# Performance work log

Hardware: AMD Instinct MI355X
Metric: run time of the kernel (lower is better)

The kernel has to match this reference:

```python
import jax, jax.numpy as jnp
import numpy as np

B, S, D, H = 4, 1024, 1024, 16
DH = D // H


def setup_inputs() -> dict:
    key = jax.random.key(0)
    ks = jax.random.split(key, 9)
    s = 0.02
    return {
        "x": jax.random.normal(ks[0], (B, S, D), dtype=jnp.float32),
        "mask": jax.random.randint(ks[1], (B, 1, S), 0, 2, dtype=jnp.int32),
        "Wq": jax.random.normal(ks[2], (D, D), dtype=jnp.float32) * s,
        "bq": jnp.zeros((D,), dtype=jnp.float32),
        "Wk": jax.random.normal(ks[3], (D, D), dtype=jnp.float32) * s,
        "Wv": jax.random.normal(ks[4], (D, D), dtype=jnp.float32) * s,
        "bv": jnp.zeros((D,), dtype=jnp.float32),
        "Wo": jax.random.normal(ks[5], (D, D), dtype=jnp.float32) * s,
        "bo": jnp.zeros((D,), dtype=jnp.float32),
    }


def reference(x, mask, Wq, bq, Wk, Wv, bv, Wo, bo):
    # Linear projections (torch Linear: y = x @ W.T + b)
    q = x @ Wq.T + bq
    k = x @ Wk.T  # key has bias=False
    v = x @ Wv.T + bv

    scale = jnp.asarray(DH, x.dtype) ** (-0.25)
    # [B,S,D] -> [B,H,S,DH]
    qh = q.reshape(B, S, H, DH).transpose(0, 2, 1, 3) * scale
    kh = k.reshape(B, S, H, DH).transpose(0, 2, 1, 3) * scale
    vh = v.reshape(B, S, H, DH).transpose(0, 2, 1, 3)

    qk = jnp.einsum("bhqd,bhkd->bhqk", qh, kh)  # [B,H,S,S]

    # pad-mask branch: mask [B,1,S] -> [B,1,1,S], 0 means padded
    pad = (mask == 0)[:, :, None, :]
    min_value = jnp.finfo(qk.dtype).min
    qk = jnp.where(pad, min_value, qk)

    qk = qk.astype(jnp.float32)
    w = jax.nn.softmax(qk, axis=-1).astype(x.dtype)
    w = jnp.where(pad, jnp.asarray(0.0, w.dtype), w)

    wv = jnp.einsum("bhqk,bhkd->bhqd", w, vh)  # [B,H,S,DH]
    wv = wv.transpose(0, 2, 1, 3).reshape(B, S, D)
    out = wv @ Wo.T + bo
    return out, jax.lax.stop_gradient(qk)
```

## Files before the change

kernel.cpp:

```cpp
#include <hip/hip_runtime.h>

#define NB 4
#define NS 1024
#define ND 1024
#define NH 16
#define NDH 64

typedef __attribute__((ext_vector_type(8))) short short8;
typedef __attribute__((ext_vector_type(4))) short s16x4;
typedef __attribute__((ext_vector_type(4))) float f32x4;

#define SENT (-3.3895313892515355e38f)

static __device__ __forceinline__ unsigned short f2bf(float f) {
    unsigned u = __builtin_bit_cast(unsigned, f);
    u += 0x7fffu + ((u >> 16) & 1u);
    return (unsigned short)(u >> 16);
}

static __device__ __forceinline__ f32x4 mfma16(short8 a, short8 b, f32x4 c) {
    return __builtin_amdgcn_mfma_f32_16x16x32_bf16(a, b, c, 0, 0, 0);
}

typedef const __attribute__((address_space(1))) unsigned int gu32_t;
typedef __attribute__((address_space(3))) unsigned int su32_t;
#define GLOAD_LDS16(gp, lp) \
    __builtin_amdgcn_global_load_lds((gu32_t*)(const void*)(gp), (su32_t*)(void*)(lp), 16, 0, 0)

__global__ __launch_bounds__(256) void cast_to_bf16(
    const float* __restrict__ x,  const float* __restrict__ wq,
    const float* __restrict__ wk, const float* __restrict__ wv,
    const float* __restrict__ wo, short* __restrict__ xb,
    short* __restrict__ wqb, short* __restrict__ wkb,
    short* __restrict__ wvb, short* __restrict__ wob)
{
    int i = blockIdx.x * 256 + threadIdx.x;
    const float* s; short* d; int off;
    const int XQ = 1 << 20, WQ = 1 << 18;
    if (i < XQ)               { s = x;  d = xb;  off = i; }
    else if (i < XQ + WQ)     { s = wq; d = wqb; off = i - XQ; }
    else if (i < XQ + 2 * WQ) { s = wk; d = wkb; off = i - XQ - WQ; }
    else if (i < XQ + 3 * WQ) { s = wv; d = wvb; off = i - XQ - 2 * WQ; }
    else                      { s = wo; d = wob; off = i - XQ - 3 * WQ; }
    float4 v = ((const float4*)s)[off];
    s16x4 r = { (short)f2bf(v.x), (short)f2bf(v.y), (short)f2bf(v.z), (short)f2bf(v.w) };
    ((s16x4*)d)[off] = r;
}

__global__ __launch_bounds__(256) void gemm_qkv(
    const short* __restrict__ X, const short* __restrict__ Wq,
    const short* __restrict__ Wk, const short* __restrict__ Wv,
    const float* __restrict__ bq, const float* __restrict__ bv,
    short* __restrict__ qd, short* __restrict__ kd, short* __restrict__ vtd)
{
    __shared__ short As[128 * 64];
    __shared__ short Bs[128 * 64];
    const int z = blockIdx.z;
    const short* W = (z == 0) ? Wq : (z == 1) ? Wk : Wv;
    const float* bias = (z == 0) ? bq : (z == 1) ? (const float*)nullptr : bv;
    const float scale = (z == 2) ? 1.0f : 0.35355339059327373f;

    const int tid = threadIdx.x;
    const int w = tid >> 6, l = tid & 63;
    const int lg = l >> 4, lc = l & 15;
    const int wr = w >> 1, wc = w & 1;
    const int bm = blockIdx.x, bn = blockIdx.y;
    const int K = ND;

    const f32x4 zf = {0.f, 0.f, 0.f, 0.f};
    f32x4 acc[4][4];
#pragma unroll
    for (int a = 0; a < 4; ++a)
#pragma unroll
        for (int b2 = 0; b2 < 4; ++b2) acc[a][b2] = zf;

    for (int t = 0; t < 16; ++t) {
        const int k0 = t * 64;
        __syncthreads();
#pragma unroll
        for (int i = 0; i < 4; ++i) {
            int lin = i * 256 + tid;
            int row = lin >> 3, cp = lin & 7;
            int c = cp ^ (row & 7);
            GLOAD_LDS16(X + (size_t)(bm * 128 + row) * K + k0 + c * 8, As + lin * 8);
            GLOAD_LDS16(W + (size_t)(bn * 128 + row) * K + k0 + c * 8, Bs + lin * 8);
        }
        __syncthreads();

        short8 af[4][2], bfr[4][2];
#pragma unroll
        for (int mb = 0; mb < 4; ++mb) {
            int r = wr * 64 + mb * 16 + lc;
#pragma unroll
            for (int ks = 0; ks < 2; ++ks) {
                int c = (ks * 4 + lg) ^ (r & 7);
                af[mb][ks] = *(const short8*)(As + r * 64 + c * 8);
            }
        }
#pragma unroll
        for (int nb = 0; nb < 4; ++nb) {
            int r = wc * 64 + nb * 16 + lc;
#pragma unroll
            for (int ks = 0; ks < 2; ++ks) {
                int c = (ks * 4 + lg) ^ (r & 7);
                bfr[nb][ks] = *(const short8*)(Bs + r * 64 + c * 8);
            }
        }
#pragma unroll
        for (int mb = 0; mb < 4; ++mb)
#pragma unroll
            for (int nb = 0; nb < 4; ++nb)
#pragma unroll
                for (int ks = 0; ks < 2; ++ks)
                    acc[mb][nb] = mfma16(af[mb][ks], bfr[nb][ks], acc[mb][nb]);
    }

#pragma unroll
    for (int mb = 0; mb < 4; ++mb) {
        int m0 = bm * 128 + wr * 64 + mb * 16 + lg * 4;
        int b = m0 >> 10, s0 = m0 & 1023;
#pragma unroll
        for (int nb = 0; nb < 4; ++nb) {
            int n = bn * 128 + wc * 64 + nb * 16 + lc;
            int h = (n >> 6) & 15, d = n & 63;
            float bv_ = bias ? bias[n] : 0.f;
            if (z == 2) {
                s16x4 pk;
#pragma unroll
                for (int r = 0; r < 4; ++r) pk[r] = (short)f2bf(acc[mb][nb][r] + bv_);
                *(s16x4*)(vtd + (((size_t)(b * NH + h) * NDH + d) * NS + s0)) = pk;
            } else {
                short* dst = (z == 0) ? qd : kd;
#pragma unroll
                for (int r = 0; r < 4; ++r) {
                    float v = (acc[mb][nb][r] + bv_) * scale;
                    ((unsigned short*)dst)[(((size_t)(b * NH + h) * NS) + s0 + r) * NDH + d] =
                        f2bf(v);
                }
            }
        }
    }
}

static __device__ __forceinline__ void stage_ab(
    const short* __restrict__ X, const short* __restrict__ W,
    int bm, int bn, int t, int tid, short* Asb, short* Bsb)
{
    const int k0 = t * 64;
#pragma unroll
    for (int i = 0; i < 4; ++i) {
        int lin = i * 256 + tid;
        int row = lin >> 3, cp = lin & 7;
        int c = cp ^ (row & 7);
        GLOAD_LDS16(X + (size_t)(bm * 128 + row) * ND + k0 + c * 8, Asb + lin * 8);
        GLOAD_LDS16(W + (size_t)(bn * 128 + row) * ND + k0 + c * 8, Bsb + lin * 8);
    }
}

static __device__ __forceinline__ void kstep128(
    const short* Asb, const short* Bsb, int wr, int wc, int lg, int lc,
    f32x4 acc[4][4])
{
    short8 af[4][2], bfr[4][2];
#pragma unroll
    for (int mb = 0; mb < 4; ++mb) {
        int r = wr * 64 + mb * 16 + lc;
#pragma unroll
        for (int ks = 0; ks < 2; ++ks) {
            int c = (ks * 4 + lg) ^ (r & 7);
            af[mb][ks] = *(const short8*)(Asb + r * 64 + c * 8);
        }
    }
#pragma unroll
    for (int nb = 0; nb < 4; ++nb) {
        int r = wc * 64 + nb * 16 + lc;
#pragma unroll
        for (int ks = 0; ks < 2; ++ks) {
            int c = (ks * 4 + lg) ^ (r & 7);
            bfr[nb][ks] = *(const short8*)(Bsb + r * 64 + c * 8);
        }
    }
#pragma unroll
    for (int mb = 0; mb < 4; ++mb)
#pragma unroll
        for (int nb = 0; nb < 4; ++nb)
#pragma unroll
            for (int ks = 0; ks < 2; ++ks)
                acc[mb][nb] = mfma16(af[mb][ks], bfr[nb][ks], acc[mb][nb]);
}

__global__ __launch_bounds__(256) void gemm_out(
    const short* __restrict__ X, const short* __restrict__ W,
    const float* __restrict__ bias, float* __restrict__ outp)
{
    __shared__ short As0[128 * 64], As1[128 * 64];
    __shared__ short Bs0[128 * 64], Bs1[128 * 64];
    const int tid = threadIdx.x;
    const int w = tid >> 6, l = tid & 63;
    const int lg = l >> 4, lc = l & 15;
    const int wr = w >> 1, wc = w & 1;
    const int bm = blockIdx.x, bn = blockIdx.y;

    const f32x4 zf = {0.f, 0.f, 0.f, 0.f};
    f32x4 acc[4][4];
#pragma unroll
    for (int a = 0; a < 4; ++a)
#pragma unroll
        for (int b2 = 0; b2 < 4; ++b2) acc[a][b2] = zf;

    stage_ab(X, W, bm, bn, 0, tid, As0, Bs0);
    __syncthreads();
    for (int t = 0; t < 16; t += 2) {
        if (t + 1 < 16) stage_ab(X, W, bm, bn, t + 1, tid, As1, Bs1);
        kstep128(As0, Bs0, wr, wc, lg, lc, acc);
        __syncthreads();
        if (t + 2 < 16) stage_ab(X, W, bm, bn, t + 2, tid, As0, Bs0);
        kstep128(As1, Bs1, wr, wc, lg, lc, acc);
        __syncthreads();
    }

#pragma unroll
    for (int mb = 0; mb < 4; ++mb) {
        int m0 = bm * 128 + wr * 64 + mb * 16 + lg * 4;
#pragma unroll
        for (int nb = 0; nb < 4; ++nb) {
            int n = bn * 128 + wc * 64 + nb * 16 + lc;
            float bv_ = bias[n];
#pragma unroll
            for (int r = 0; r < 4; ++r)
                outp[(size_t)(m0 + r) * ND + n] = acc[mb][nb][r] + bv_;
        }
    }
}

static __device__ __forceinline__ void stage_kv(
    const short* __restrict__ kb, const short* __restrict__ vt,
    int bh, int t, int tid, short* Ksb, short* Vsb)
{
#pragma unroll
    for (int i = 0; i < 2; ++i) {
        int lin = i * 256 + tid;
        int row = lin >> 3, cp = lin & 7;
        int c = cp ^ (row & 7);
        GLOAD_LDS16(kb + ((size_t)(bh * NS + t * 64 + row)) * NDH + c * 8, Ksb + lin * 8);
        GLOAD_LDS16(vt + ((size_t)(bh * NDH + row)) * NS + t * 64 + c * 8, Vsb + lin * 8);
    }
}

__global__ __launch_bounds__(256) void attn_mfma(
    const short* __restrict__ qb, const short* __restrict__ kb,
    const short* __restrict__ vt, const int* __restrict__ mask,
    float* __restrict__ qk_out, unsigned short* __restrict__ wv_out)
{
    __shared__ short Ks0[64 * 64], Ks1[64 * 64];
    __shared__ short Vs0[64 * 64], Vs1[64 * 64];
    __shared__ short Ps[4][16 * 68];
    __shared__ int Msk[NS];
    const int qt = blockIdx.x, bh = blockIdx.y;
    const int b = bh >> 4, h = bh & 15;
    const int q0 = qt * 64;
    const int tid = threadIdx.x;
    const int w = tid >> 6, l = tid & 63;
    const int lg = l >> 4, lc = l & 15;

#pragma unroll
    for (int i = 0; i < 4; ++i) Msk[i * 256 + tid] = mask[b * NS + i * 256 + tid];

    short8 aq[2];
    {
        const short* qrow = qb + ((size_t)(bh * NS + q0 + w * 16 + lc)) * NDH;
#pragma unroll
        for (int ks = 0; ks < 2; ++ks) aq[ks] = *(const short8*)(qrow + ks * 32 + lg * 8);
    }

    const f32x4 zf = {0.f, 0.f, 0.f, 0.f};
    f32x4 o[4];
    float mr = -INFINITY, lr = 0.f;
#pragma unroll
    for (int db = 0; db < 4; ++db) o[db] = zf;

    const size_t qrowbase = (size_t)(bh * NS + q0 + w * 16 + lc) * NS;

    stage_kv(kb, vt, bh, 0, tid, Ks0, Vs0);
    __syncthreads();

#pragma unroll
    for (int t2 = 0; t2 < 16; t2 += 2) {
#pragma unroll
        for (int half = 0; half < 2; ++half) {
            const int t = t2 + half;
            const short* Ksc = half ? Ks1 : Ks0;
            const short* Vsc = half ? Vs1 : Vs0;
            if (t + 1 < 16)
                stage_kv(kb, vt, bh, t + 1, tid, half ? Ks0 : Ks1, half ? Vs0 : Vs1);

            f32x4 s[4];
#pragma unroll
            for (int jb = 0; jb < 4; ++jb) {
                s[jb] = zf;
#pragma unroll
                for (int ks = 0; ks < 2; ++ks) {
                    int rk = jb * 16 + lc;
                    int c = (ks * 4 + lg) ^ (rk & 7);
                    short8 kf = *(const short8*)(Ksc + rk * 64 + c * 8);
                    s[jb] = mfma16(kf, aq[ks], s[jb]);
                }
            }

            float sm[4][4];
#pragma unroll
            for (int jb = 0; jb < 4; ++jb) {
                int4 mi = *(const int4*)(Msk + t * 64 + jb * 16 + lg * 4);
                f32x4 sv;
                sv[0] = mi.x ? s[jb][0] : SENT;
                sv[1] = mi.y ? s[jb][1] : SENT;
                sv[2] = mi.z ? s[jb][2] : SENT;
                sv[3] = mi.w ? s[jb][3] : SENT;
                __builtin_nontemporal_store(
                    sv, (f32x4*)(qk_out + qrowbase + t * 64 + jb * 16 + lg * 4));
                sm[jb][0] = mi.x ? s[jb][0] : -INFINITY;
                sm[jb][1] = mi.y ? s[jb][1] : -INFINITY;
                sm[jb][2] = mi.z ? s[jb][2] : -INFINITY;
                sm[jb][3] = mi.w ? s[jb][3] : -INFINITY;
            }

            float pm = -INFINITY;
#pragma unroll
            for (int jb = 0; jb < 4; ++jb)
                pm = fmaxf(pm, fmaxf(fmaxf(sm[jb][0], sm[jb][1]),
                                     fmaxf(sm[jb][2], sm[jb][3])));
            pm = fmaxf(pm, __shfl_xor(pm, 16));
            pm = fmaxf(pm, __shfl_xor(pm, 32));

            float nm = fmaxf(mr, pm);
            float f = (nm == -INFINITY) ? 1.f : __expf(mr - nm);
            float nms = (nm == -INFINITY) ? 0.f : nm;
            mr = nm;

            float p[4][4], ps = 0.f;
#pragma unroll
            for (int jb = 0; jb < 4; ++jb)
#pragma unroll
                for (int r = 0; r < 4; ++r) {
                    float e = __expf(sm[jb][r] - nms);
                    p[jb][r] = e;
                    ps += e;
                }
            ps += __shfl_xor(ps, 16);
            ps += __shfl_xor(ps, 32);
            lr = lr * f + ps;

            f32x4 fv;
#pragma unroll
            for (int r = 0; r < 4; ++r) fv[r] = __shfl(f, lg * 4 + r, 16);
#pragma unroll
            for (int db = 0; db < 4; ++db) o[db] *= fv;

#pragma unroll
            for (int jb = 0; jb < 4; ++jb) {
                s16x4 pk;
#pragma unroll
                for (int r = 0; r < 4; ++r) pk[r] = (short)f2bf(p[jb][r]);
                *(s16x4*)(&Ps[w][lc * 68 + jb * 16 + lg * 4]) = pk;
            }
            short8 pa[2];
#pragma unroll
            for (int ks = 0; ks < 2; ++ks)
                pa[ks] = *(const short8*)(&Ps[w][lc * 68 + ks * 32 + lg * 8]);

#pragma unroll
            for (int db = 0; db < 4; ++db)
#pragma unroll
                for (int ks = 0; ks < 2; ++ks) {
                    int rv = db * 16 + lc;
                    int c = (ks * 4 + lg) ^ (rv & 7);
                    short8 bvf = *(const short8*)(Vsc + rv * 64 + c * 8);
                    o[db] = mfma16(pa[ks], bvf, o[db]);
                }

            __syncthreads();
        }
    }

    float inv = (lr > 0.f) ? 1.f / lr : 0.f;
    f32x4 invv;
#pragma unroll
    for (int r = 0; r < 4; ++r) invv[r] = __shfl(inv, lg * 4 + r, 16);
#pragma unroll
    for (int db = 0; db < 4; ++db)
#pragma unroll
        for (int r = 0; r < 4; ++r) {
            float v = o[db][r] * invv[r];
            wv_out[(((size_t)(b * NS + q0 + w * 16 + lg * 4 + r)) * NH + h) * NDH + db * 16 + lc] =
                f2bf(v);
        }
}

extern "C" void kernel_launch(void* const* d_in, const int* in_sizes, int n_in,
                              void* d_out, int out_size, void* d_ws, size_t ws_size,
                              hipStream_t stream) {
    const float* x    = (const float*)d_in[0];
    const int*   mask = (const int*)d_in[1];
    const float* Wq   = (const float*)d_in[2];
    const float* bq   = (const float*)d_in[3];
    const float* Wk   = (const float*)d_in[4];
    const float* Wv   = (const float*)d_in[5];
    const float* bv   = (const float*)d_in[6];
    const float* Wo   = (const float*)d_in[7];
    const float* bo   = (const float*)d_in[8];

    float* out    = (float*)d_out;
    float* qk_out = out + (size_t)NB * NS * ND;

    const size_t MI = 1u << 20;
    short* xb  = (short*)d_ws;
    short* wqb = xb  + 4 * MI;
    short* wkb = wqb + MI;
    short* wvb = wkb + MI;
    short* wob = wvb + MI;
    short* qbf = wob + MI;
    short* kbf = qbf + 4 * MI;
    short* vtb = kbf + 4 * MI;
    short* wvo = vtb + 4 * MI;

    cast_to_bf16<<<8192, 256, 0, stream>>>(x, Wq, Wk, Wv, Wo, xb, wqb, wkb, wvb, wob);

    dim3 blk(256);
    dim3 qgrid(32, 8, 3);
    gemm_qkv<<<qgrid, blk, 0, stream>>>(xb, wqb, wkb, wvb, bq, bv, qbf, kbf, vtb);

    dim3 agrid(16, 64);
    attn_mfma<<<agrid, blk, 0, stream>>>(qbf, kbf, vtb, mask, qk_out, (unsigned short*)wvo);

    dim3 ogrid(32, 8);
    gemm_out<<<ogrid, blk, 0, stream>>>(wvo, wob, bo, out);
}
```

Baseline: 421.4 us.

## Load K/V fragments directly from global memory, dropping LDS staging and block barriers

Removes the double-buffered LDS staging of K and V tiles and the shared mask copy; each wave now reads its MFMA K/V fragments and mask values straight from global memory, with no __syncthreads in the loop. Launch bounds now request 4 blocks per SM, relying on the smaller LDS footprint for higher occupancy. The aim is to cut LDS traffic and barrier stalls. In exchange the four waves of a block each fetch the same K/V data from global memory, so reuse depends on the cache, and there is no explicit prefetch overlap.

```diff
diff --git a/kernel.cpp b/kernel.cpp
--- a/kernel.cpp
+++ b/kernel.cpp
@@ -233,29 +233,12 @@
     }
 }
 
-static __device__ __forceinline__ void stage_kv(
-    const short* __restrict__ kb, const short* __restrict__ vt,
-    int bh, int t, int tid, short* Ksb, short* Vsb)
-{
-#pragma unroll
-    for (int i = 0; i < 2; ++i) {
-        int lin = i * 256 + tid;
-        int row = lin >> 3, cp = lin & 7;
-        int c = cp ^ (row & 7);
-        GLOAD_LDS16(kb + ((size_t)(bh * NS + t * 64 + row)) * NDH + c * 8, Ksb + lin * 8);
-        GLOAD_LDS16(vt + ((size_t)(bh * NDH + row)) * NS + t * 64 + c * 8, Vsb + lin * 8);
-    }
-}
-
-__global__ __launch_bounds__(256) void attn_mfma(
+__global__ __launch_bounds__(256, 4) void attn_mfma(
     const short* __restrict__ qb, const short* __restrict__ kb,
     const short* __restrict__ vt, const int* __restrict__ mask,
     float* __restrict__ qk_out, unsigned short* __restrict__ wv_out)
 {
-    __shared__ short Ks0[64 * 64], Ks1[64 * 64];
-    __shared__ short Vs0[64 * 64], Vs1[64 * 64];
     __shared__ short Ps[4][16 * 68];
-    __shared__ int Msk[NS];
     const int qt = blockIdx.x, bh = blockIdx.y;
     const int b = bh >> 4, h = bh & 15;
     const int q0 = qt * 64;
@@ -263,122 +246,97 @@
     const int w = tid >> 6, l = tid & 63;
     const int lg = l >> 4, lc = l & 15;
 
-#pragma unroll
-    for (int i = 0; i < 4; ++i) Msk[i * 256 + tid] = mask[b * NS + i * 256 + tid];
-
-    short8 aq[2];
+    short8 aq0, aq1;
     {
         const short* qrow = qb + ((size_t)(bh * NS + q0 + w * 16 + lc)) * NDH;
-#pragma unroll
-        for (int ks = 0; ks < 2; ++ks) aq[ks] = *(const short8*)(qrow + ks * 32 + lg * 8);
+        aq0 = *(const short8*)(qrow + lg * 8);
+        aq1 = *(const short8*)(qrow + 32 + lg * 8);
     }
 
     const f32x4 zf = {0.f, 0.f, 0.f, 0.f};
     f32x4 o[4];
+#pragma unroll
+    for (int db = 0; db < 4; ++db) o[db] = zf;
     float mr = -INFINITY, lr = 0.f;
-#pragma unroll
-    for (int db = 0; db < 4; ++db) o[db] = zf;
 
     const size_t qrowbase = (size_t)(bh * NS + q0 + w * 16 + lc) * NS;
-
-    stage_kv(kb, vt, bh, 0, tid, Ks0, Vs0);
-    __syncthreads();
-
-#pragma unroll
-    for (int t2 = 0; t2 < 16; t2 += 2) {
-#pragma unroll
-        for (int half = 0; half < 2; ++half) {
-            const int t = t2 + half;
-            const short* Ksc = half ? Ks1 : Ks0;
-            const short* Vsc = half ? Vs1 : Vs0;
-            if (t + 1 < 16)
-                stage_kv(kb, vt, bh, t + 1, tid, half ? Ks0 : Ks1, half ? Vs0 : Vs1);
-
-            f32x4 s[4];
-#pragma unroll
-            for (int jb = 0; jb < 4; ++jb) {
-                s[jb] = zf;
-#pragma unroll
-                for (int ks = 0; ks < 2; ++ks) {
-                    int rk = jb * 16 + lc;
-                    int c = (ks * 4 + lg) ^ (rk & 7);
-                    short8 kf = *(const short8*)(Ksc + rk * 64 + c * 8);
-                    s[jb] = mfma16(kf, aq[ks], s[jb]);
-                }
+    const short* kbase = kb + (size_t)bh * NS * NDH;
+    const short* vbase = vt + (size_t)bh * NDH * NS;
+    const int* mbase = mask + b * NS;
+    short* psw = &Ps[w][0];
+
+    for (int t = 0; t < 16; ++t) {
+        f32x4 s[4];
+#pragma unroll
+        for (int jb = 0; jb < 4; ++jb) {
+            const short* kr = kbase + (size_t)(t * 64 + jb * 16 + lc) * NDH + lg * 8;
+            s[jb] = mfma16(*(const short8*)kr, aq0, zf);
+            s[jb] = mfma16(*(const short8*)(kr + 32), aq1, s[jb]);
+        }
+
+#pragma unroll
+        for (int jb = 0; jb < 4; ++jb) {
+            int4 mi = *(const int4*)(mbase + t * 64 + jb * 16 + lg * 4);
+            f32x4 sv;
+            sv[0] = mi.x ? s[jb][0] : SENT;
+            sv[1] = mi.y ? s[jb][1] : SENT;
+            sv[2] = mi.z ? s[jb][2] : SENT;
+            sv[3] = mi.w ? s[jb][3] : SENT;
+            __builtin_nontemporal_store(
+                sv, (f32x4*)(qk_out + qrowbase + t * 64 + jb * 16 + lg * 4));
+            s[jb][0] = mi.x ? s[jb][0] : -INFINITY;
+            s[jb][1] = mi.y ? s[jb][1] : -INFINITY;
+            s[jb][2] = mi.z ? s[jb][2] : -INFINITY;
+            s[jb][3] = mi.w ? s[jb][3] : -INFINITY;
+        }
+
+        float pm = -INFINITY;
+#pragma unroll
+        for (int jb = 0; jb < 4; ++jb)
+            pm = fmaxf(pm, fmaxf(fmaxf(s[jb][0], s[jb][1]),
+                                 fmaxf(s[jb][2], s[jb][3])));
+        pm = fmaxf(pm, __shfl_xor(pm, 16));
+        pm = fmaxf(pm, __shfl_xor(pm, 32));
+
+        float nm = fmaxf(mr, pm);
+        float f = (nm == -INFINITY) ? 1.f : __expf(mr - nm);
+        float nms = (nm == -INFINITY) ? 0.f : nm;
+        mr = nm;
+
+        float p[4][4], ps_ = 0.f;
+#pragma unroll
+        for (int jb = 0; jb < 4; ++jb)
+#pragma unroll
+            for (int r = 0; r < 4; ++r) {
+                float e = __expf(s[jb][r] - nms);
+                p[jb][r] = e;
+                ps_ += e;
             }
-
-            float sm[4][4];
-#pragma unroll
-            for (int jb = 0; jb < 4; ++jb) {
-                int4 mi = *(const int4*)(Msk + t * 64 + jb * 16 + lg * 4);
-                f32x4 sv;
-                sv[0] = mi.x ? s[jb][0] : SENT;
-                sv[1] = mi.y ? s[jb][1] : SENT;
-                sv[2] = mi.z ? s[jb][2] : SENT;
-                sv[3] = mi.w ? s[jb][3] : SENT;
-                __builtin_nontemporal_store(
-                    sv, (f32x4*)(qk_out + qrowbase + t * 64 + jb * 16 + lg * 4));
-                sm[jb][0] = mi.x ? s[jb][0] : -INFINITY;
-                sm[jb][1] = mi.y ? s[jb][1] : -INFINITY;
-                sm[jb][2] = mi.z ? s[jb][2] : -INFINITY;
-                sm[jb][3] = mi.w ? s[jb][3] : -INFINITY;
-            }
-
-            float pm = -INFINITY;
-#pragma unroll
-            for (int jb = 0; jb < 4; ++jb)
-                pm = fmaxf(pm, fmaxf(fmaxf(sm[jb][0], sm[jb][1]),
-                                     fmaxf(sm[jb][2], sm[jb][3])));
-            pm = fmaxf(pm, __shfl_xor(pm, 16));
-            pm = fmaxf(pm, __shfl_xor(pm, 32));
-
-            float nm = fmaxf(mr, pm);
-            float f = (nm == -INFINITY) ? 1.f : __expf(mr - nm);
-            float nms = (nm == -INFINITY) ? 0.f : nm;
-            mr = nm;
-
-            float p[4][4], ps = 0.f;
-#pragma unroll
-            for (int jb = 0; jb < 4; ++jb)
-#pragma unroll
-                for (int r = 0; r < 4; ++r) {
-                    float e = __expf(sm[jb][r] - nms);
-                    p[jb][r] = e;
-                    ps += e;
-                }
-            ps += __shfl_xor(ps, 16);
-            ps += __shfl_xor(ps, 32);
-            lr = lr * f + ps;
-
-            f32x4 fv;
-#pragma unroll
-            for (int r = 0; r < 4; ++r) fv[r] = __shfl(f, lg * 4 + r, 16);
-#pragma unroll
-            for (int db = 0; db < 4; ++db) o[db] *= fv;
-
-#pragma unroll
-            for (int jb = 0; jb < 4; ++jb) {
-                s16x4 pk;
-#pragma unroll
-                for (int r = 0; r < 4; ++r) pk[r] = (short)f2bf(p[jb][r]);
-                *(s16x4*)(&Ps[w][lc * 68 + jb * 16 + lg * 4]) = pk;
-            }
-            short8 pa[2];
-#pragma unroll
-            for (int ks = 0; ks < 2; ++ks)
-                pa[ks] = *(const short8*)(&Ps[w][lc * 68 + ks * 32 + lg * 8]);
-
-#pragma unroll
-            for (int db = 0; db < 4; ++db)
-#pragma unroll
-                for (int ks = 0; ks < 2; ++ks) {
-                    int rv = db * 16 + lc;
-                    int c = (ks * 4 + lg) ^ (rv & 7);
-                    short8 bvf = *(const short8*)(Vsc + rv * 64 + c * 8);
-                    o[db] = mfma16(pa[ks], bvf, o[db]);
-                }
-
-            __syncthreads();
+        ps_ += __shfl_xor(ps_, 16);
+        ps_ += __shfl_xor(ps_, 32);
+        lr = lr * f + ps_;
+
+        f32x4 fv;
+#pragma unroll
+        for (int r = 0; r < 4; ++r) fv[r] = __shfl(f, lg * 4 + r, 16);
+#pragma unroll
+        for (int db = 0; db < 4; ++db) o[db] *= fv;
+
+#pragma unroll
+        for (int jb = 0; jb < 4; ++jb) {
+            s16x4 pk;
+#pragma unroll
+            for (int r = 0; r < 4; ++r) pk[r] = (short)f2bf(p[jb][r]);
+            *(s16x4*)(psw + lc * 68 + jb * 16 + lg * 4) = pk;
+        }
+        short8 pa0 = *(const short8*)(psw + lc * 68 + lg * 8);
+        short8 pa1 = *(const short8*)(psw + lc * 68 + 32 + lg * 8);
+
+#pragma unroll
+        for (int db = 0; db < 4; ++db) {
+            const short* vr = vbase + (size_t)(db * 16 + lc) * NS + t * 64 + lg * 8;
+            o[db] = mfma16(pa0, *(const short8*)vr, o[db]);
+            o[db] = mfma16(pa1, *(const short8*)(vr + 32), o[db]);
         }
     }
 
```

Result: slower. 472.9 us (+12.2%).
